# Kernel tuning notes

Hardware: AMD Instinct MI355X
Metric: run time of the kernel (lower is better)

## Reference

```python
import jax, jax.numpy as jnp
import numpy as np

ALPHA = 0.9
BETA = 0.85
THRESHOLD = 1.0
SIM_TIME = 128  # simulation_time
SURR_SCALE = 100.0


@jax.custom_vjp
def spike(x):
    # Heaviside step (SurrGradSpike.forward)
    return (x > 0).astype(x.dtype)

def _spike_fwd(x):
    return spike(x), x

def _spike_bwd(x, g):
    # fast-sigmoid surrogate gradient (Zenke & Ganguli 2018)
    return (g / (SURR_SCALE * jnp.abs(x) + 1.0) ** 2,)

spike.defvjp(_spike_fwd, _spike_bwd)


def setup_inputs() -> dict:
    key = jax.random.key(0)
    k0, k1, k2, k3 = jax.random.split(key, 4)
    B, IN, H = 16384, 128, 512
    inputs = jax.random.normal(k0, (B, IN), dtype=jnp.float32)
    # architecture[0] is doubled by the pos/neg input split -> W0: [2*IN, H]
    W0 = jax.random.normal(k1, (2 * IN, H), dtype=jnp.float32)
    W1 = jax.random.normal(k2, (H, H), dtype=jnp.float32)
    W2 = jax.random.normal(k3, (H, H), dtype=jnp.float32)
    return {"inputs": inputs, "W0": W0, "W1": W1, "W2": W2}


def _forward(inputs, Ws):
    # split input into positive / rectified-negative halves, concat on feature dim
    x = jnp.concatenate([jnp.maximum(inputs, 0.0), jnp.maximum(-inputs, 0.0)], axis=1)
    B = x.shape[0]
    L = len(Ws)
    syn0 = tuple(jnp.zeros((B, W.shape[1]), x.dtype) for W in Ws)
    mem0 = tuple(jnp.zeros((B, W.shape[1]), x.dtype) for W in Ws)

    def step(carry, _):
        syn, mem = carry
        new_syn, new_mem = [], []
        prev_spk = None
        for l, W in enumerate(Ws):
            h = jnp.einsum("bi,ij->bj", x if l == 0 else prev_spk, W)
            s = h if l == 0 else ALPHA * syn[l] + h  # layer 0: 0*syn + h
            m = BETA * mem[l] + s
            if l < L - 1:
                mthr = m - THRESHOLD
                prev_spk = spike(mthr)
                m = jnp.where(mthr > 0, 0.0, m)  # reset spiked membranes
            new_syn.append(s)
            new_mem.append(m)
        return (tuple(new_syn), tuple(new_mem)), None

    # t=0 in the original only records zeros and skips the update -> run T-1 steps
    (syn, mem), _ = jax.lax.scan(step, (syn0, mem0), None, length=SIM_TIME - 1)
    # returned value = mem_rec[-1][-1]: last layer membrane at final timestep
    return mem[-1]


def reference(inputs, W0, W1, W2):
    return _forward(inputs, (W0, W1, W2))
```

## Files before the change

kernel.cpp:

```cpp
#include <hip/hip_runtime.h>
#include <stdint.h>


typedef __attribute__((ext_vector_type(2))) float f32x2;
typedef __attribute__((ext_vector_type(4))) float f32x4;

#define ALPHA 0.9f
#define BETA 0.85f
#define NSTEPS 127
#define WGT 1024
#define ROWS 32
#define CPAD 36
#define HPAD 516

#define LIF_L0(M, H, SP) { float _m = BETA * (M) + (H); \
    const bool _b = (_m - 1.0f) > 0.0f; (M) = _b ? 0.0f : _m; \
    (SP) = _b ? 1.0f : 0.0f; }
#define LIF_MID(S, M, A, SP) { (S) = ALPHA * (S) + (A); \
    float _m = BETA * (M) + (S); const bool _b = (_m - 1.0f) > 0.0f; \
    (M) = _b ? 0.0f : _m; (SP) = _b ? 1.0f : 0.0f; }
#define LIF_OUT(S, M, A) { (S) = ALPHA * (S) + (A); (M) = BETA * (M) + (S); }

__global__ __launch_bounds__(WGT, 4)
void dsnn_kernel(const float* __restrict__ x,
                 const float* __restrict__ W0,
                 const float* __restrict__ W1,
                 const float* __restrict__ W2,
                 float* __restrict__ out)
{
    __shared__ float spkbuf[512 * CPAD];
    __shared__ float h0buf[ROWS * HPAD];

    const int t  = threadIdx.x;
    const int c2 = (t & 255) * 2;
    const int g  = (t >> 8) * 8;
    const int r0 = blockIdx.x * ROWS;

    for (int k = t; k < 256 * ROWS; k += WGT) {
        const int i = k >> 5;
        const int r = k & 31;
        const float v = (i < 128) ? x[(size_t)(r0 + r) * 128 + i]
                                  : -x[(size_t)(r0 + r) * 128 + (i - 128)];
        spkbuf[i * CPAD + r] = fmaxf(v, 0.0f);
    }
    __syncthreads();

    f32x2 acc2[8];

    auto gemm = [&](const float* Wcol, int K) {
        #pragma unroll 2
        for (int j = 0; j < K; ++j) {
            const float* sb = spkbuf + j * CPAD + g;
            const f32x4 sA = *(const f32x4*)(sb);
            const f32x4 sB = *(const f32x4*)(sb + 4);
            const f32x2 wv = *(const f32x2*)(Wcol + (size_t)j * 512);
            f32x2 a01 = { sA[0], sA[1] };
            f32x2 a23 = { sA[2], sA[3] };
            f32x2 b01 = { sB[0], sB[1] };
            f32x2 b23 = { sB[2], sB[3] };
            asm("v_pk_fma_f32 %0, %8, %12, %0 op_sel:[0,0,0] op_sel_hi:[0,1,1]\n\t"
                "v_pk_fma_f32 %1, %8, %12, %1 op_sel:[1,0,0] op_sel_hi:[1,1,1]\n\t"
                "v_pk_fma_f32 %2, %9, %12, %2 op_sel:[0,0,0] op_sel_hi:[0,1,1]\n\t"
                "v_pk_fma_f32 %3, %9, %12, %3 op_sel:[1,0,0] op_sel_hi:[1,1,1]\n\t"
                "v_pk_fma_f32 %4, %10, %12, %4 op_sel:[0,0,0] op_sel_hi:[0,1,1]\n\t"
                "v_pk_fma_f32 %5, %10, %12, %5 op_sel:[1,0,0] op_sel_hi:[1,1,1]\n\t"
                "v_pk_fma_f32 %6, %11, %12, %6 op_sel:[0,0,0] op_sel_hi:[0,1,1]\n\t"
                "v_pk_fma_f32 %7, %11, %12, %7 op_sel:[1,0,0] op_sel_hi:[1,1,1]"
                : "+v"(acc2[0]), "+v"(acc2[1]), "+v"(acc2[2]), "+v"(acc2[3]),
                  "+v"(acc2[4]), "+v"(acc2[5]), "+v"(acc2[6]), "+v"(acc2[7])
                : "v"(a01), "v"(a23), "v"(b01), "v"(b23), "v"(wv));
        }
    };

    #pragma unroll
    for (int r = 0; r < 8; ++r) acc2[r] = (f32x2){ 0.0f, 0.0f };
    gemm(W0 + c2, 256);
    #pragma unroll
    for (int r = 0; r < 8; ++r)
        *(f32x2*)(h0buf + (g + r) * HPAD + c2) = acc2[r];
    __syncthreads();

    float m0[8][2], s1[8][2], m1[8][2], s2[8][2], m2[8][2];
    #pragma unroll
    for (int r = 0; r < 8; ++r)
        #pragma unroll
        for (int cc = 0; cc < 2; ++cc) {
            m0[r][cc] = 0.f; s1[r][cc] = 0.f; m1[r][cc] = 0.f;
            s2[r][cc] = 0.f; m2[r][cc] = 0.f;
        }

    for (int step = 0; step < NSTEPS; ++step) {
        {
            f32x4 svA[2], svB[2];
            #pragma unroll
            for (int rr = 0; rr < 4; ++rr) {
                const f32x2 hva = *(const f32x2*)(h0buf + (g + rr) * HPAD + c2);
                const f32x2 hvb = *(const f32x2*)(h0buf + (g + 4 + rr) * HPAD + c2);
                LIF_L0(m0[rr][0], hva.x, svA[0][rr]);
                LIF_L0(m0[rr][1], hva.y, svA[1][rr]);
                LIF_L0(m0[4 + rr][0], hvb.x, svB[0][rr]);
                LIF_L0(m0[4 + rr][1], hvb.y, svB[1][rr]);
            }
            #pragma unroll
            for (int cc = 0; cc < 2; ++cc) {
                *(f32x4*)(spkbuf + (c2 + cc) * CPAD + g)     = svA[cc];
                *(f32x4*)(spkbuf + (c2 + cc) * CPAD + g + 4) = svB[cc];
            }
        }
        __syncthreads();

        #pragma unroll
        for (int r = 0; r < 8; ++r) acc2[r] = (f32x2){ 0.0f, 0.0f };
        gemm(W1 + c2, 512);
        __syncthreads();

        {
            f32x4 svA[2], svB[2];
            #pragma unroll
            for (int rr = 0; rr < 4; ++rr) {
                LIF_MID(s1[rr][0], m1[rr][0], acc2[rr][0], svA[0][rr]);
                LIF_MID(s1[rr][1], m1[rr][1], acc2[rr][1], svA[1][rr]);
                LIF_MID(s1[4 + rr][0], m1[4 + rr][0], acc2[4 + rr][0], svB[0][rr]);
                LIF_MID(s1[4 + rr][1], m1[4 + rr][1], acc2[4 + rr][1], svB[1][rr]);
            }
            #pragma unroll
            for (int cc = 0; cc < 2; ++cc) {
                *(f32x4*)(spkbuf + (c2 + cc) * CPAD + g)     = svA[cc];
                *(f32x4*)(spkbuf + (c2 + cc) * CPAD + g + 4) = svB[cc];
            }
        }
        __syncthreads();

        #pragma unroll
        for (int r = 0; r < 8; ++r) acc2[r] = (f32x2){ 0.0f, 0.0f };
        gemm(W2 + c2, 512);
        #pragma unroll
        for (int r = 0; r < 8; ++r) {
            LIF_OUT(s2[r][0], m2[r][0], acc2[r][0]);
            LIF_OUT(s2[r][1], m2[r][1], acc2[r][1]);
        }
        __syncthreads();
    }

    #pragma unroll
    for (int r = 0; r < 8; ++r) {
        f32x2 ov = { m2[r][0], m2[r][1] };
        *(f32x2*)(out + (size_t)(r0 + g + r) * 512 + c2) = ov;
    }
}

extern "C" void kernel_launch(void* const* d_in, const int* in_sizes, int n_in,
                              void* d_out, int out_size, void* d_ws, size_t ws_size,
                              hipStream_t stream) {
    const float* inputs = (const float*)d_in[0];
    const float* W0     = (const float*)d_in[1];
    const float* W1     = (const float*)d_in[2];
    const float* W2     = (const float*)d_in[3];
    float* out          = (float*)d_out;

    dim3 grid(16384 / ROWS);
    dim3 block(WGT);
    dsnn_kernel<<<grid, block, 0, stream>>>(inputs, W0, W1, W2, out);
}
```

Baseline: 33.03 ms.

## Widen per-thread register tile to 8x4 with half the threads

Halves the workgroup to 512 threads and has each thread compute 8 rows by 4 columns instead of 8 by 2. The GEMM now issues 16 packed FMAs per k step from one f32x4 weight load and two f32x4 spike loads, raising arithmetic per LDS and global load. In exchange, per-thread state arrays double, which raises register pressure and lowers occupancy (launch bounds change from 4 to 2).

```diff
diff --git a/kernel.cpp b/kernel.cpp
--- a/kernel.cpp
+++ b/kernel.cpp
@@ -8,7 +8,7 @@
 #define ALPHA 0.9f
 #define BETA 0.85f
 #define NSTEPS 127
-#define WGT 1024
+#define WGT 512
 #define ROWS 32
 #define CPAD 36
 #define HPAD 516
@@ -21,7 +21,30 @@
     (M) = _b ? 0.0f : _m; (SP) = _b ? 1.0f : 0.0f; }
 #define LIF_OUT(S, M, A) { (S) = ALPHA * (S) + (A); (M) = BETA * (M) + (S); }
 
-__global__ __launch_bounds__(WGT, 4)
+#define PK16(Q0, Q1, Q2, Q3, W01, W23) \
+    asm("v_pk_fma_f32 %0, %16, %20, %0 op_sel:[0,0,0] op_sel_hi:[1,0,1]\n\t" \
+        "v_pk_fma_f32 %1, %16, %20, %1 op_sel:[0,1,0] op_sel_hi:[1,1,1]\n\t" \
+        "v_pk_fma_f32 %2, %16, %21, %2 op_sel:[0,0,0] op_sel_hi:[1,0,1]\n\t" \
+        "v_pk_fma_f32 %3, %16, %21, %3 op_sel:[0,1,0] op_sel_hi:[1,1,1]\n\t" \
+        "v_pk_fma_f32 %4, %17, %20, %4 op_sel:[0,0,0] op_sel_hi:[1,0,1]\n\t" \
+        "v_pk_fma_f32 %5, %17, %20, %5 op_sel:[0,1,0] op_sel_hi:[1,1,1]\n\t" \
+        "v_pk_fma_f32 %6, %17, %21, %6 op_sel:[0,0,0] op_sel_hi:[1,0,1]\n\t" \
+        "v_pk_fma_f32 %7, %17, %21, %7 op_sel:[0,1,0] op_sel_hi:[1,1,1]\n\t" \
+        "v_pk_fma_f32 %8, %18, %20, %8 op_sel:[0,0,0] op_sel_hi:[1,0,1]\n\t" \
+        "v_pk_fma_f32 %9, %18, %20, %9 op_sel:[0,1,0] op_sel_hi:[1,1,1]\n\t" \
+        "v_pk_fma_f32 %10, %18, %21, %10 op_sel:[0,0,0] op_sel_hi:[1,0,1]\n\t" \
+        "v_pk_fma_f32 %11, %18, %21, %11 op_sel:[0,1,0] op_sel_hi:[1,1,1]\n\t" \
+        "v_pk_fma_f32 %12, %19, %20, %12 op_sel:[0,0,0] op_sel_hi:[1,0,1]\n\t" \
+        "v_pk_fma_f32 %13, %19, %20, %13 op_sel:[0,1,0] op_sel_hi:[1,1,1]\n\t" \
+        "v_pk_fma_f32 %14, %19, %21, %14 op_sel:[0,0,0] op_sel_hi:[1,0,1]\n\t" \
+        "v_pk_fma_f32 %15, %19, %21, %15 op_sel:[0,1,0] op_sel_hi:[1,1,1]" \
+        : "+v"(acc[0][0]), "+v"(acc[0][1]), "+v"(acc[0][2]), "+v"(acc[0][3]), \
+          "+v"(acc[1][0]), "+v"(acc[1][1]), "+v"(acc[1][2]), "+v"(acc[1][3]), \
+          "+v"(acc[2][0]), "+v"(acc[2][1]), "+v"(acc[2][2]), "+v"(acc[2][3]), \
+          "+v"(acc[3][0]), "+v"(acc[3][1]), "+v"(acc[3][2]), "+v"(acc[3][3]) \
+        : "v"(Q0), "v"(Q1), "v"(Q2), "v"(Q3), "v"(W01), "v"(W23))
+
+__global__ __launch_bounds__(WGT, 2)
 void dsnn_kernel(const float* __restrict__ x,
                  const float* __restrict__ W0,
                  const float* __restrict__ W1,
@@ -32,8 +55,8 @@
     __shared__ float h0buf[ROWS * HPAD];
 
     const int t  = threadIdx.x;
-    const int c2 = (t & 255) * 2;
-    const int g  = (t >> 8) * 8;
+    const int c4 = (t & 127) * 4;
+    const int g  = (t >> 7) * 8;
     const int r0 = blockIdx.x * ROWS;
 
     for (int k = t; k < 256 * ROWS; k += WGT) {
@@ -45,107 +68,112 @@
     }
     __syncthreads();
 
-    f32x2 acc2[8];
+    f32x2 acc[4][4];
 
-    auto gemm = [&](const float* Wcol, int K) {
+    auto gemm = [&](const float* Wbase, int K) {
         #pragma unroll 2
         for (int j = 0; j < K; ++j) {
             const float* sb = spkbuf + j * CPAD + g;
             const f32x4 sA = *(const f32x4*)(sb);
             const f32x4 sB = *(const f32x4*)(sb + 4);
-            const f32x2 wv = *(const f32x2*)(Wcol + (size_t)j * 512);
-            f32x2 a01 = { sA[0], sA[1] };
-            f32x2 a23 = { sA[2], sA[3] };
-            f32x2 b01 = { sB[0], sB[1] };
-            f32x2 b23 = { sB[2], sB[3] };
-            asm("v_pk_fma_f32 %0, %8, %12, %0 op_sel:[0,0,0] op_sel_hi:[0,1,1]\n\t"
-                "v_pk_fma_f32 %1, %8, %12, %1 op_sel:[1,0,0] op_sel_hi:[1,1,1]\n\t"
-                "v_pk_fma_f32 %2, %9, %12, %2 op_sel:[0,0,0] op_sel_hi:[0,1,1]\n\t"
-                "v_pk_fma_f32 %3, %9, %12, %3 op_sel:[1,0,0] op_sel_hi:[1,1,1]\n\t"
-                "v_pk_fma_f32 %4, %10, %12, %4 op_sel:[0,0,0] op_sel_hi:[0,1,1]\n\t"
-                "v_pk_fma_f32 %5, %10, %12, %5 op_sel:[1,0,0] op_sel_hi:[1,1,1]\n\t"
-                "v_pk_fma_f32 %6, %11, %12, %6 op_sel:[0,0,0] op_sel_hi:[0,1,1]\n\t"
-                "v_pk_fma_f32 %7, %11, %12, %7 op_sel:[1,0,0] op_sel_hi:[1,1,1]"
-                : "+v"(acc2[0]), "+v"(acc2[1]), "+v"(acc2[2]), "+v"(acc2[3]),
-                  "+v"(acc2[4]), "+v"(acc2[5]), "+v"(acc2[6]), "+v"(acc2[7])
-                : "v"(a01), "v"(a23), "v"(b01), "v"(b23), "v"(wv));
+            const f32x4 wv = *(const f32x4*)(Wbase + (size_t)j * 512 + c4);
+            f32x2 q0 = { sA[0], sA[1] };
+            f32x2 q1 = { sA[2], sA[3] };
+            f32x2 q2 = { sB[0], sB[1] };
+            f32x2 q3 = { sB[2], sB[3] };
+            f32x2 w01 = { wv[0], wv[1] };
+            f32x2 w23 = { wv[2], wv[3] };
+            PK16(q0, q1, q2, q3, w01, w23);
         }
     };
 
     #pragma unroll
-    for (int r = 0; r < 8; ++r) acc2[r] = (f32x2){ 0.0f, 0.0f };
-    gemm(W0 + c2, 256);
+    for (int p = 0; p < 4; ++p)
+        #pragma unroll
+        for (int cc = 0; cc < 4; ++cc) acc[p][cc] = (f32x2){0.f, 0.f};
+    gemm(W0, 256);
     #pragma unroll
-    for (int r = 0; r < 8; ++r)
-        *(f32x2*)(h0buf + (g + r) * HPAD + c2) = acc2[r];
+    for (int r = 0; r < 8; ++r) {
+        f32x4 hv = { acc[r >> 1][0][r & 1], acc[r >> 1][1][r & 1],
+                     acc[r >> 1][2][r & 1], acc[r >> 1][3][r & 1] };
+        *(f32x4*)(h0buf + (g + r) * HPAD + c4) = hv;
+    }
     __syncthreads();
 
-    float m0[8][2], s1[8][2], m1[8][2], s2[8][2], m2[8][2];
+    float m0[8][4], s1[8][4], m1[8][4], s2[8][4], m2[8][4];
     #pragma unroll
     for (int r = 0; r < 8; ++r)
         #pragma unroll
-        for (int cc = 0; cc < 2; ++cc) {
+        for (int cc = 0; cc < 4; ++cc) {
             m0[r][cc] = 0.f; s1[r][cc] = 0.f; m1[r][cc] = 0.f;
             s2[r][cc] = 0.f; m2[r][cc] = 0.f;
         }
 
     for (int step = 0; step < NSTEPS; ++step) {
         {
-            f32x4 svA[2], svB[2];
+            f32x4 svA[4], svB[4];
             #pragma unroll
             for (int rr = 0; rr < 4; ++rr) {
-                const f32x2 hva = *(const f32x2*)(h0buf + (g + rr) * HPAD + c2);
-                const f32x2 hvb = *(const f32x2*)(h0buf + (g + 4 + rr) * HPAD + c2);
-                LIF_L0(m0[rr][0], hva.x, svA[0][rr]);
-                LIF_L0(m0[rr][1], hva.y, svA[1][rr]);
-                LIF_L0(m0[4 + rr][0], hvb.x, svB[0][rr]);
-                LIF_L0(m0[4 + rr][1], hvb.y, svB[1][rr]);
+                const f32x4 hva = *(const f32x4*)(h0buf + (g + rr) * HPAD + c4);
+                const f32x4 hvb = *(const f32x4*)(h0buf + (g + 4 + rr) * HPAD + c4);
+                #pragma unroll
+                for (int cc = 0; cc < 4; ++cc) {
+                    LIF_L0(m0[rr][cc], hva[cc], svA[cc][rr]);
+                    LIF_L0(m0[4 + rr][cc], hvb[cc], svB[cc][rr]);
+                }
             }
             #pragma unroll
-            for (int cc = 0; cc < 2; ++cc) {
-                *(f32x4*)(spkbuf + (c2 + cc) * CPAD + g)     = svA[cc];
-                *(f32x4*)(spkbuf + (c2 + cc) * CPAD + g + 4) = svB[cc];
+            for (int cc = 0; cc < 4; ++cc) {
+                *(f32x4*)(spkbuf + (c4 + cc) * CPAD + g)     = svA[cc];
+                *(f32x4*)(spkbuf + (c4 + cc) * CPAD + g + 4) = svB[cc];
             }
         }
         __syncthreads();
 
         #pragma unroll
-        for (int r = 0; r < 8; ++r) acc2[r] = (f32x2){ 0.0f, 0.0f };
-        gemm(W1 + c2, 512);
+        for (int p = 0; p < 4; ++p)
+            #pragma unroll
+            for (int cc = 0; cc < 4; ++cc) acc[p][cc] = (f32x2){0.f, 0.f};
+        gemm(W1, 512);
         __syncthreads();
 
         {
-            f32x4 svA[2], svB[2];
+            f32x4 svA[4], svB[4];
             #pragma unroll
             for (int rr = 0; rr < 4; ++rr) {
-                LIF_MID(s1[rr][0], m1[rr][0], acc2[rr][0], svA[0][rr]);
-                LIF_MID(s1[rr][1], m1[rr][1], acc2[rr][1], svA[1][rr]);
-                LIF_MID(s1[4 + rr][0], m1[4 + rr][0], acc2[4 + rr][0], svB[0][rr]);
-                LIF_MID(s1[4 + rr][1], m1[4 + rr][1], acc2[4 + rr][1], svB[1][rr]);
+                #pragma unroll
+                for (int cc = 0; cc < 4; ++cc) {
+                    LIF_MID(s1[rr][cc], m1[rr][cc],
+                            acc[rr >> 1][cc][rr & 1], svA[cc][rr]);
+                    LIF_MID(s1[4 + rr][cc], m1[4 + rr][cc],
+                            acc[(4 + rr) >> 1][cc][rr & 1], svB[cc][rr]);
+                }
             }
             #pragma unroll
-            for (int cc = 0; cc < 2; ++cc) {
-                *(f32x4*)(spkbuf + (c2 + cc) * CPAD + g)     = svA[cc];
-                *(f32x4*)(spkbuf + (c2 + cc) * CPAD + g + 4) = svB[cc];
+            for (int cc = 0; cc < 4; ++cc) {
+                *(f32x4*)(spkbuf + (c4 + cc) * CPAD + g)     = svA[cc];
+                *(f32x4*)(spkbuf + (c4 + cc) * CPAD + g + 4) = svB[cc];
             }
         }
         __syncthreads();
 
         #pragma unroll
-        for (int r = 0; r < 8; ++r) acc2[r] = (f32x2){ 0.0f, 0.0f };
-        gemm(W2 + c2, 512);
+        for (int p = 0; p < 4; ++p)
+            #pragma unroll
+            for (int cc = 0; cc < 4; ++cc) acc[p][cc] = (f32x2){0.f, 0.f};
+        gemm(W2, 512);
         #pragma unroll
-        for (int r = 0; r < 8; ++r) {
-            LIF_OUT(s2[r][0], m2[r][0], acc2[r][0]);
-            LIF_OUT(s2[r][1], m2[r][1], acc2[r][1]);
-        }
+        for (int r = 0; r < 8; ++r)
+            #pragma unroll
+            for (int cc = 0; cc < 4; ++cc)
+                LIF_OUT(s2[r][cc], m2[r][cc], acc[r >> 1][cc][r & 1]);
         __syncthreads();
     }
 
     #pragma unroll
     for (int r = 0; r < 8; ++r) {
-        f32x2 ov = { m2[r][0], m2[r][1] };
-        *(f32x2*)(out + (size_t)(r0 + g + r) * 512 + c2) = ov;
+        f32x4 ov = { m2[r][0], m2[r][1], m2[r][2], m2[r][3] };
+        *(f32x4*)(out + (size_t)(r0 + g + r) * 512 + c4) = ov;
     }
 }
 
```

Result: faster. 30.93 ms (median of 2 runs) (-6.3%).
